# Optimization experiments

Measured on AMD Instinct MI355X. Metric: run time of the kernel, lower is better.

## Reference

```python
import jax, jax.numpy as jnp
import numpy as np

BS, L, S, AMB = 64, 64, 63, 32   # batch, sentence len, opseq steps, ambiguities per step
H, E, V, MLP = 128, 300, 50000, 1024
EPS = 1e-8


def setup_inputs() -> dict:
    key = jax.random.key(0)
    ks = jax.random.split(key, 12)
    u = lambda k, shp: jax.random.uniform(k, shp, dtype=jnp.float32) * 0.1
    return {
        "sentences1": jax.random.randint(ks[0], (BS, L), 0, V, dtype=jnp.int32),
        "operations1": jax.random.randint(ks[1], (BS, S, 2 * AMB), 0, L, dtype=jnp.int32),
        "oopl1": jnp.full((BS,), L + S, dtype=jnp.int32),
        "sentences2": jax.random.randint(ks[2], (BS, L), 0, V, dtype=jnp.int32),
        "operations2": jax.random.randint(ks[3], (BS, S, 2 * AMB), 0, L, dtype=jnp.int32),
        "oopl2": jnp.full((BS,), L + S, dtype=jnp.int32),
        "W": u(ks[4], (5 * H, E)),
        "U": u(ks[5], (5 * H, 2 * H)),
        "b": jnp.zeros((5 * H,), dtype=jnp.float32),
        "energy_u": u(ks[6], (H,)),
        "unk_embedding": u(ks[7], (E,)),
        "word_embeddings": jax.random.normal(ks[8], (V, E), dtype=jnp.float32),
        "A": u(ks[9], (MLP, 4 * H)),
        "a": u(ks[10], (MLP,)),
        "inv_temperature": jnp.float32(1.0),
    }


def _gates(preact, ccL, ccR):
    # preact: [..., 5H]; tree-LSTM cell (i, fL, fR, o, u gates)
    i = jax.nn.sigmoid(preact[..., :H])
    fL = jax.nn.sigmoid(preact[..., H:2 * H])
    fR = jax.nn.sigmoid(preact[..., 2 * H:3 * H])
    o = jax.nn.sigmoid(preact[..., 3 * H:4 * H])
    u = jnp.tanh(preact[..., 4 * H:5 * H])
    c = fL * ccL + fR * ccR + i * u
    h = o * jnp.tanh(c)
    return c, h


def _run_chart(sentences, operations, W, U, b, energy_u, unk_embedding,
               word_embeddings, inv_temperature):
    bs = sentences.shape[0]
    # leaf phase: embed each word, preact = W @ emb + b, ccL = ccR = 0
    emb = jnp.where(sentences[..., None] >= 0,
                    word_embeddings[jnp.clip(sentences, 0)], unk_embedding)  # [bs,L,E]
    preact = jnp.einsum('ble,ge->blg', emb, W) + b                            # [bs,L,5H]
    c, h = _gates(preact, 0.0, 0.0)
    chart = jnp.zeros((bs, L + S, 2 * H), dtype=jnp.float32)
    chart = chart.at[:, :L, :].set(jnp.concatenate([c, h], axis=-1))

    def step(chart, inp):
        ops, pos = inp                                   # ops: [bs, 2*AMB], pos: scalar
        entries = jnp.take_along_axis(chart, ops[:, :, None].astype(jnp.int32), axis=1)
        entries = entries.reshape(bs, AMB, 2, 2 * H)     # [bs, amb, (L,R), 2H]
        ccL = entries[:, :, 0, :H]
        ccR = entries[:, :, 1, :H]
        hh = entries[:, :, :, H:].reshape(bs, AMB, 2 * H)  # concat(hL, hR)
        pre = jnp.einsum('bak,gk->bag', hh, U) + b         # [bs, amb, 5H]
        c, h = _gates(pre, ccL, ccR)
        # cosine similarity of h against energy_u
        hn = jnp.maximum(jnp.sqrt(jnp.sum(h * h, axis=-1)), EPS)
        un = jnp.maximum(jnp.sqrt(jnp.sum(energy_u * energy_u)), EPS)
        e = jnp.einsum('bah,h->ba', h, energy_u) / (hn * un)
        s = jax.nn.softmax(e * inv_temperature, axis=1)    # [bs, amb]
        combined = jnp.concatenate([jnp.einsum('ba,bah->bh', s, c),
                                    jnp.einsum('ba,bah->bh', s, h)], axis=-1)
        chart = jax.lax.dynamic_update_slice(chart, combined[:, None, :], (0, pos, 0))
        return chart, None

    ops_seq = jnp.swapaxes(operations, 0, 1)             # [S, bs, 2*AMB]
    positions = L + jnp.arange(S, dtype=jnp.int32)
    chart, _ = jax.lax.scan(step, chart, (ops_seq, positions))
    return chart


def reference(sentences1, operations1, oopl1, sentences2, operations2, oopl2,
              W, U, b, energy_u, unk_embedding, word_embeddings, A, a,
              inv_temperature):
    chart1 = _run_chart(sentences1, operations1, W, U, b, energy_u,
                        unk_embedding, word_embeddings, inv_temperature)
    chart2 = _run_chart(sentences2, operations2, W, U, b, energy_u,
                        unk_embedding, word_embeddings, inv_temperature)
    bs = chart1.shape[0]
    bidx = jnp.arange(bs)
    s1 = chart1[bidx, oopl1 - 1, H:]                     # final composed h, [bs, H]
    s2 = chart2[bidx, oopl2 - 1, H:]
    u = (s1 - s2) ** 2
    v = s1 * s2
    conc = jnp.concatenate([u, v, s1, s2], axis=1)       # [bs, 4H]
    out = jax.nn.relu(jnp.einsum('jk,ik->ij', A, conc) + a)
    return out
```

## Files before the change

kernel.cpp:

```cpp
#include <hip/hip_runtime.h>
#include <hip/hip_bf16.h>

#define BSZ 64
#define LL  64
#define SS  63
#define AMB 32
#define HH  128
#define EE  300
#define MLPN 1024
#define GG  640
#define K2  256
#define PP  127
#define CCS 36

typedef __attribute__((ext_vector_type(8))) short short8;
typedef __attribute__((ext_vector_type(4))) float f32x4;

__device__ __forceinline__ float sigf(float x) { return 1.f / (1.f + __expf(-x)); }

__device__ __forceinline__ unsigned short f2bf(float x) {
    unsigned int u = __float_as_uint(x);
    u += 0x7fffu + ((u >> 16) & 1u);
    return (unsigned short)(u >> 16);
}

#define PW 25600
#define PU 20480
#define PZ 129024
__global__ void __launch_bounds__(256) prep_kernel(
        const float* __restrict__ W, const float* __restrict__ U,
        const int* __restrict__ ops1, const int* __restrict__ ops2,
        const int* __restrict__ oopl1, const int* __restrict__ oopl2,
        short* __restrict__ WTB, short* __restrict__ UTB,
        float* __restrict__ chart,
        int* __restrict__ live_list, int* __restrict__ nlive_bar) {
    __shared__ unsigned char live[2][64];
    const int tid = threadIdx.x;

    if (blockIdx.x == gridDim.x - 1) {
        if (tid < 128) live[tid >> 6][tid & 63] = 0;
        __syncthreads();
        if (tid < BSZ) {
            int p1 = oopl1[tid] - 1;
            if (p1 >= LL && p1 < PP) live[0][p1 - LL] = 1;
            int p2 = oopl2[tid] - 1;
            if (p2 >= LL && p2 < PP) live[1][p2 - LL] = 1;
        }
        __syncthreads();
        for (int t = SS - 1; t >= 1; --t) {
            if (live[0][t]) {
                for (int i = tid; i < BSZ * 2 * AMB; i += 256) {
                    int p = ops1[((i >> 6) * SS + t) * 64 + (i & 63)];
                    if (p >= LL && p < PP) live[0][p - LL] = 1;
                }
            }
            if (live[1][t]) {
                for (int i = tid; i < BSZ * 2 * AMB; i += 256) {
                    int p = ops2[((i >> 6) * SS + t) * 64 + (i & 63)];
                    if (p >= LL && p < PP) live[1][p - LL] = 1;
                }
            }
            __syncthreads();
        }
        if (tid == 0) {
            int n = 0;
            for (int t = 0; t < SS; ++t) {
                int f = (live[0][t] ? 1 : 0) | (live[1][t] ? 2 : 0);
                if (f) live_list[n++] = t | (f << 8);
            }
            nlive_bar[0] = n;
            nlive_bar[1] = 0;
        }
        return;
    }

    int idx = blockIdx.x * 256 + tid;
    if (idx < PW) {
        int lane = idx & 63, r = idx >> 6;
        int kk = r % 10, n = r / 10;
        int g = n * 16 + (lane & 15);
        int k0 = kk * 32 + ((lane >> 4) << 3);
        const float* src = W + (size_t)g * EE + k0;
        float f[8];
        if (k0 + 8 <= EE) {
            f32x4 x0 = *(const f32x4*)src;
            f32x4 x1 = *(const f32x4*)(src + 4);
            f[0]=x0[0]; f[1]=x0[1]; f[2]=x0[2]; f[3]=x0[3];
            f[4]=x1[0]; f[5]=x1[1]; f[6]=x1[2]; f[7]=x1[3];
        } else {
#pragma unroll
            for (int j = 0; j < 8; ++j) f[j] = (k0 + j < EE) ? src[j] : 0.f;
        }
        short8 v;
#pragma unroll
        for (int j = 0; j < 8; ++j) v[j] = (short)f2bf(f[j]);
        *(short8*)(WTB + (size_t)idx * 8) = v;
    } else if (idx < PW + PU) {
        int o = idx - PW;
        int lane = o & 63, r = o >> 6;
        int kk = r & 7, n = r >> 3;
        int g = n * 16 + (lane & 15);
        int k0 = kk * 32 + ((lane >> 4) << 3);
        const float* src = U + (size_t)g * K2 + k0;
        f32x4 x0 = *(const f32x4*)src;
        f32x4 x1 = *(const f32x4*)(src + 4);
        short8 v;
        v[0]=(short)f2bf(x0[0]); v[1]=(short)f2bf(x0[1]); v[2]=(short)f2bf(x0[2]); v[3]=(short)f2bf(x0[3]);
        v[4]=(short)f2bf(x1[0]); v[5]=(short)f2bf(x1[1]); v[6]=(short)f2bf(x1[2]); v[7]=(short)f2bf(x1[3]);
        *(short8*)(UTB + (size_t)o * 8) = v;
    } else if (idx < PW + PU + PZ) {
        int z = idx - PW - PU;
        int row = z >> 4;
        int pair = row / 63, srow = row - pair * 63;
        float* p = chart + ((size_t)pair * PP + LL + srow) * K2 + ((z & 15) << 4);
        f32x4 zero = {0.f, 0.f, 0.f, 0.f};
        *(f32x4*)p = zero; *(f32x4*)(p+4) = zero; *(f32x4*)(p+8) = zero; *(f32x4*)(p+12) = zero;
    }
}

__global__ void __launch_bounds__(256) leaf_kernel(
        const int* __restrict__ sent1, const int* __restrict__ sent2,
        const short* __restrict__ WTB, const float* __restrict__ bias,
        const float* __restrict__ unk, const float* __restrict__ wemb,
        float* __restrict__ chart) {
    __shared__ short8 As[2 * 10 * 64];
    const int tid  = threadIdx.x;
    const int tok0 = blockIdx.x * 32;
    const int* sent = (blockIdx.x >= 128) ? sent2 : sent1;

    float f[5][8];
    int ts[5], os[5];
#pragma unroll
    for (int i = 0; i < 5; ++i) {
        int slot = i * 256 + tid;
        int t = slot / 40, oct = slot - t * 40;
        ts[i] = t; os[i] = oct;
        int s = sent[(tok0 + t) & 4095];
        const float* src = (s >= 0) ? (wemb + (size_t)s * EE) : unk;
        int k0 = oct * 8;
        if (k0 + 8 <= EE) {
            f32x4 x0 = *(const f32x4*)(src + k0);
            f32x4 x1 = *(const f32x4*)(src + k0 + 4);
            f[i][0]=x0[0]; f[i][1]=x0[1]; f[i][2]=x0[2]; f[i][3]=x0[3];
            f[i][4]=x1[0]; f[i][5]=x1[1]; f[i][6]=x1[2]; f[i][7]=x1[3];
        } else {
#pragma unroll
            for (int j = 0; j < 8; ++j) f[i][j] = (k0 + j < EE) ? src[k0 + j] : 0.f;
        }
    }
#pragma unroll
    for (int i = 0; i < 5; ++i) {
        int t = ts[i], oct = os[i];
        short8 v;
#pragma unroll
        for (int j = 0; j < 8; ++j) v[j] = (short)f2bf(f[i][j]);
        As[((t >> 4) * 10 + (oct >> 2)) * 64 + ((oct & 3) << 4) + (t & 15)] = v;
    }
    __syncthreads();

    const int w = tid >> 6, lane = tid & 63;
    const int quad = lane >> 4, l15 = lane & 15;
    for (int cc = 0; cc < 2; ++cc) {
        int nu = cc * 4 + w;
        f32x4 acc[2][3] = {};
        for (int kk = 0; kk < 10; ++kk) {
            short8 a0 = As[kk * 64 + lane];
            short8 a1 = As[(10 + kk) * 64 + lane];
#pragma unroll
            for (int si = 0; si < 3; ++si) {
                int s5 = (si == 0) ? 0 : (si == 1 ? 3 : 4);
                short8 bv = *(const short8*)(WTB + ((size_t)((nu + 8 * s5) * 10 + kk) * 64 + lane) * 8);
                acc[0][si] = __builtin_amdgcn_mfma_f32_16x16x32_bf16(a0, bv, acc[0][si], 0, 0, 0);
                acc[1][si] = __builtin_amdgcn_mfma_f32_16x16x32_bf16(a1, bv, acc[1][si], 0, 0, 0);
            }
        }
        int jc = nu * 16 + l15;
        float bi = bias[jc], bo = bias[384 + jc], bu = bias[512 + jc];
#pragma unroll
        for (int mt = 0; mt < 2; ++mt)
#pragma unroll
        for (int r = 0; r < 4; ++r) {
            float pi = acc[mt][0][r] + bi;
            float po = acc[mt][1][r] + bo;
            float pu = acc[mt][2][r] + bu;
            float cv = sigf(pi) * tanhf(pu);
            float hv = sigf(po) * tanhf(cv);
            int tok = tok0 + mt * 16 + quad * 4 + r;
            float* dst = chart + ((size_t)(tok >> 6) * PP + (tok & 63)) * K2;
            dst[jc]      = cv;
            dst[HH + jc] = hv;
        }
    }
}

#define GRID_STEP 512
__device__ __forceinline__ void gbar(int* bar, int gen) {
    __syncthreads();
    if (threadIdx.x == 0) {
        __threadfence();
        __hip_atomic_fetch_add(bar, 1, __ATOMIC_ACQ_REL, __HIP_MEMORY_SCOPE_AGENT);
        while (__hip_atomic_load(bar, __ATOMIC_ACQUIRE, __HIP_MEMORY_SCOPE_AGENT) < gen * GRID_STEP)
            __builtin_amdgcn_s_sleep(2);
        __threadfence();
    }
    __syncthreads();
}

__global__ void __launch_bounds__(256, 2) step_kernel(
        const int* __restrict__ ops1, const int* __restrict__ ops2,
        const short* __restrict__ UTB, const float* __restrict__ bias,
        const float* __restrict__ eu, const float* __restrict__ invt,
        float* __restrict__ chart,
        const int* __restrict__ live_list, int* __restrict__ nlive_bar,
        float* __restrict__ e_scr) {
    __shared__ __align__(16) char smem[16384 + 4 * (32 * CCS * 4)];
    short8* As2 = (short8*)smem;
    float* ccL = (float*)(smem + 16384);
    float* ccR = (float*)(smem + 16384 + 4608);
    float* chc = (float*)(smem + 16384 + 2 * 4608);
    float* chh = (float*)(smem + 16384 + 3 * 4608);
    __shared__ int ops_lds[64];
    __shared__ float s_w[AMB];
    __shared__ float un_sh;

    const int tid = threadIdx.x;
    const int pair = blockIdx.x >> 2, slice = blockIdx.x & 3;
    const int ch = pair >> 6, b = pair & 63;
    const int* ops = ch ? ops2 : ops1;
    float* chbase = chart + (size_t)pair * PP * K2;
    const float it = invt[0];
    const int w = tid >> 6, lane = tid & 63, quad = lane >> 4, l15 = lane & 15;
    const int mt = w >> 1, nul = w & 1, nu = slice * 2 + nul;
    const int jc = nu * 16 + l15, lc = nul * 16 + l15;
    const float bi  = bias[jc],          bfl = bias[HH + jc];
    const float bfr = bias[2 * HH + jc], bo  = bias[3 * HH + jc];
    const float bu  = bias[4 * HH + jc];
    const float euc = eu[slice * 32 + (lane & 31)];

    if (tid < 64) {
        float v = eu[tid] * eu[tid] + eu[tid + 64] * eu[tid + 64];
        for (int off = 32; off >= 1; off >>= 1) v += __shfl_xor(v, off);
        if (tid == 0) un_sh = fmaxf(sqrtf(v), 1e-8f);
    }
    __syncthreads();

    const int nl = nlive_bar[0];
    int* bar = nlive_bar + 1;
    int gen = 0;

    for (int sidx = 0; sidx < nl; ++sidx) {
        int entry = live_list[sidx];
        int t = entry & 0xff;
        bool active = (entry >> (8 + ch)) & 1;

        if (active) {
            if (tid < 64) ops_lds[tid] = min(max(ops[(b * SS + t) * 64 + tid], 0), PP - 1);
            __syncthreads();

            float hf[4][8];
            int ha[4], ho[4];
#pragma unroll
            for (int i = 0; i < 4; ++i) {
                int s = i * 256 + tid;
                int a = s >> 5, oct = s & 31, side = oct >> 4, m8 = oct & 15;
                ha[i] = a; ho[i] = oct;
                const float* src = chbase + (size_t)ops_lds[2 * a + side] * K2 + HH + m8 * 8;
                f32x4 x0 = *(const f32x4*)src;
                f32x4 x1 = *(const f32x4*)(src + 4);
                hf[i][0]=x0[0]; hf[i][1]=x0[1]; hf[i][2]=x0[2]; hf[i][3]=x0[3];
                hf[i][4]=x1[0]; hf[i][5]=x1[1]; hf[i][6]=x1[2]; hf[i][7]=x1[3];
            }
            f32x4 cv4[2];
            int ca[2], cq[2], cs[2];
#pragma unroll
            for (int i = 0; i < 2; ++i) {
                int s2 = i * 256 + tid;
                int a = s2 >> 4, rest = s2 & 15, side = rest >> 3, qi = rest & 7;
                ca[i] = a; cq[i] = qi; cs[i] = side;
                cv4[i] = *(const f32x4*)(chbase + (size_t)ops_lds[2 * a + side] * K2 + slice * 32 + qi * 4);
            }
#pragma unroll
            for (int i = 0; i < 4; ++i) {
                short8 v;
#pragma unroll
                for (int j = 0; j < 8; ++j) v[j] = (short)f2bf(hf[i][j]);
                As2[((ha[i] >> 4) * 8 + (ho[i] >> 2)) * 64 + ((ho[i] & 3) << 4) + (ha[i] & 15)] = v;
            }
#pragma unroll
            for (int i = 0; i < 2; ++i) {
                float* dst = (cs[i] ? ccR : ccL) + ca[i] * CCS + cq[i] * 4;
                *(f32x4*)dst = cv4[i];
            }
            __syncthreads();

            f32x4 acc[5] = {};
            for (int kk = 0; kk < 8; ++kk) {
                short8 a0 = As2[(mt * 8 + kk) * 64 + lane];
#pragma unroll
                for (int s5 = 0; s5 < 5; ++s5) {
                    short8 bb = *(const short8*)(UTB + ((size_t)((nu + 8 * s5) * 8 + kk) * 64 + lane) * 8);
                    acc[s5] = __builtin_amdgcn_mfma_f32_16x16x32_bf16(a0, bb, acc[s5], 0, 0, 0);
                }
            }
#pragma unroll
            for (int r = 0; r < 4; ++r) {
                int a = mt * 16 + quad * 4 + r;
                float cv = sigf(acc[1][r] + bfl) * ccL[a * CCS + lc]
                         + sigf(acc[2][r] + bfr) * ccR[a * CCS + lc]
                         + sigf(acc[0][r] + bi) * tanhf(acc[4][r] + bu);
                float hv = sigf(acc[3][r] + bo) * tanhf(cv);
                chc[a * CCS + lc] = cv;
                chh[a * CCS + lc] = hv;
            }
            __syncthreads();

#pragma unroll
            for (int ii = 0; ii < 4; ++ii) {
                int a = w * 8 + ii * 2 + (lane >> 5);
                float hv = chh[a * CCS + (lane & 31)];
                float pe = hv * euc, pn = hv * hv;
                for (int off = 16; off >= 1; off >>= 1) {
                    pe += __shfl_xor(pe, off);
                    pn += __shfl_xor(pn, off);
                }
                if ((lane & 31) == 0) {
                    float* d = e_scr + ((size_t)(pair * 4 + slice) * 32 + a) * 2;
                    d[0] = pe; d[1] = pn;
                }
            }
        }

        ++gen; gbar(bar, gen);

        if (active) {
            if (tid < 32) {
                const float* es = e_scr + (size_t)pair * 256 + tid * 2;
                float num = es[0] + es[64] + es[128] + es[192];
                float h2  = es[1] + es[65] + es[129] + es[193];
                float v = (num / (fmaxf(sqrtf(h2), 1e-8f) * un_sh)) * it;
                float m = v;
                for (int off = 16; off >= 1; off >>= 1) m = fmaxf(m, __shfl_xor(m, off));
                float ex = __expf(v - m);
                float su = ex;
                for (int off = 16; off >= 1; off >>= 1) su += __shfl_xor(su, off);
                s_w[tid] = ex / su;
            }
            __syncthreads();
            if (tid < 64) {
                int half = tid >> 5, lcc = tid & 31;
                const float* srcA = half ? chh : chc;
                float sacc = 0.f;
#pragma unroll
                for (int a = 0; a < AMB; ++a) sacc = fmaf(s_w[a], srcA[a * CCS + lcc], sacc);
                chbase[(size_t)(LL + t) * K2 + half * HH + slice * 32 + lcc] = sacc;
            }
            __syncthreads();
        }

        if (sidx + 1 < nl) { ++gen; gbar(bar, gen); }
    }
}

__global__ void __launch_bounds__(256) mlp_kernel(
        const float* __restrict__ chart,
        const int* __restrict__ oopl1, const int* __restrict__ oopl2,
        const float* __restrict__ A, const float* __restrict__ abias,
        float* __restrict__ out) {
    __shared__ __align__(16) float conc[4][512];
    const int tid = threadIdx.x;
    const int jt = blockIdx.x & 15, bt = blockIdx.x >> 4;

#pragma unroll
    for (int i = 0; i < 2; ++i) {
        int s = i * 256 + tid;
        int bl = s >> 7, kv = s & 127;
        int k0 = kv * 4, sel = k0 >> 7, kk0 = k0 & 127;
        int b = bt * 4 + bl;
        int p1 = min(max(oopl1[b] - 1, 0), PP - 1);
        int p2 = min(max(oopl2[b] - 1, 0), PP - 1);
        f32x4 s1 = *(const f32x4*)(chart + ((size_t)(b * PP + p1)) * K2 + HH + kk0);
        f32x4 s2 = *(const f32x4*)(chart + ((size_t)((BSZ + b) * PP + p2)) * K2 + HH + kk0);
        f32x4 v;
        if (sel == 0)      { f32x4 d = s1 - s2; v = d * d; }
        else if (sel == 1) v = s1 * s2;
        else if (sel == 2) v = s1;
        else               v = s2;
        *(f32x4*)&conc[bl][k0] = v;
    }
    __syncthreads();

    const int jj = tid & 63, bg = tid >> 6;
    const int j = jt * 64 + jj, b = bt * 4 + bg;
    const float* Arow = A + (size_t)j * 512;
    float acc0 = abias[j], acc1 = 0.f;
    for (int k = 0; k < 512; k += 8) {
        f32x4 a0 = *(const f32x4*)(Arow + k);
        f32x4 a1 = *(const f32x4*)(Arow + k + 4);
        f32x4 c0 = *(const f32x4*)&conc[bg][k];
        f32x4 c1 = *(const f32x4*)&conc[bg][k + 4];
#pragma unroll
        for (int u = 0; u < 4; ++u) {
            acc0 = fmaf(a0[u], c0[u], acc0);
            acc1 = fmaf(a1[u], c1[u], acc1);
        }
    }
    out[(size_t)b * MLPN + j] = fmaxf(acc0 + acc1, 0.f);
}

extern "C" void kernel_launch(void* const* d_in, const int* in_sizes, int n_in,
                              void* d_out, int out_size, void* d_ws, size_t ws_size,
                              hipStream_t stream) {
    const int*   sent1 = (const int*)d_in[0];
    const int*   ops1  = (const int*)d_in[1];
    const int*   oopl1 = (const int*)d_in[2];
    const int*   sent2 = (const int*)d_in[3];
    const int*   ops2  = (const int*)d_in[4];
    const int*   oopl2 = (const int*)d_in[5];
    const float* W     = (const float*)d_in[6];
    const float* U     = (const float*)d_in[7];
    const float* bias  = (const float*)d_in[8];
    const float* eu    = (const float*)d_in[9];
    const float* unk   = (const float*)d_in[10];
    const float* wemb  = (const float*)d_in[11];
    const float* A     = (const float*)d_in[12];
    const float* ab    = (const float*)d_in[13];
    const float* invt  = (const float*)d_in[14];
    float* out = (float*)d_out;
    (void)in_sizes; (void)n_in; (void)out_size; (void)ws_size;

    char* ws = (char*)d_ws;
    const size_t CHART_OFF = 0;
    const size_t WTB_OFF   = 16646144;
    const size_t UTB_OFF   = 17055744;
    const size_t LIST_OFF  = 17383424;
    const size_t NB_OFF    = 17383680;
    const size_t ESCR_OFF  = 17383936;
    float* chart     = (float*)(ws + CHART_OFF);
    short* WTB       = (short*)(ws + WTB_OFF);
    short* UTB       = (short*)(ws + UTB_OFF);
    int*   live_list = (int*)(ws + LIST_OFF);
    int*   nlive_bar = (int*)(ws + NB_OFF);
    float* e_scr     = (float*)(ws + ESCR_OFF);

    prep_kernel<<<685, 256, 0, stream>>>(W, U, ops1, ops2, oopl1, oopl2,
                                         WTB, UTB, chart, live_list, nlive_bar);

    leaf_kernel<<<256, 256, 0, stream>>>(sent1, sent2, WTB, bias, unk, wemb, chart);

    step_kernel<<<GRID_STEP, 256, 0, stream>>>(ops1, ops2, UTB, bias, eu, invt, chart,
                                               live_list, nlive_bar, e_scr);

    mlp_kernel<<<256, 256, 0, stream>>>(chart, oopl1, oopl2, A, ab, out);
}
```

Before: 214.0 us.

## Fuse leaf and step phases into one per-pair block, drop grid barriers

Replaces the leaf kernel and the grid-barrier step kernel with a single 1024-thread block per sentence pair that computes leaves, zeroes its chart rows, and runs the composition steps with only block-level syncs. Liveness analysis now runs per batch element with a 64-bit mask inside each block, rather than as a union across the batch in the prep kernel. This removes the cross-block atomic barriers and scratch traffic for the energy reduction. In exchange only 128 blocks run, so much of the GPU sits idle and each block's serial step chain is longer.

```diff
diff --git a/kernel.cpp b/kernel.cpp
--- a/kernel.cpp
+++ b/kernel.cpp
@@ -11,7 +11,6 @@
 #define GG  640
 #define K2  256
 #define PP  127
-#define CCS 36
 
 typedef __attribute__((ext_vector_type(8))) short short8;
 typedef __attribute__((ext_vector_type(4))) float f32x4;
@@ -26,55 +25,10 @@
 
 #define PW 25600
 #define PU 20480
-#define PZ 129024
 __global__ void __launch_bounds__(256) prep_kernel(
         const float* __restrict__ W, const float* __restrict__ U,
-        const int* __restrict__ ops1, const int* __restrict__ ops2,
-        const int* __restrict__ oopl1, const int* __restrict__ oopl2,
-        short* __restrict__ WTB, short* __restrict__ UTB,
-        float* __restrict__ chart,
-        int* __restrict__ live_list, int* __restrict__ nlive_bar) {
-    __shared__ unsigned char live[2][64];
-    const int tid = threadIdx.x;
-
-    if (blockIdx.x == gridDim.x - 1) {
-        if (tid < 128) live[tid >> 6][tid & 63] = 0;
-        __syncthreads();
-        if (tid < BSZ) {
-            int p1 = oopl1[tid] - 1;
-            if (p1 >= LL && p1 < PP) live[0][p1 - LL] = 1;
-            int p2 = oopl2[tid] - 1;
-            if (p2 >= LL && p2 < PP) live[1][p2 - LL] = 1;
-        }
-        __syncthreads();
-        for (int t = SS - 1; t >= 1; --t) {
-            if (live[0][t]) {
-                for (int i = tid; i < BSZ * 2 * AMB; i += 256) {
-                    int p = ops1[((i >> 6) * SS + t) * 64 + (i & 63)];
-                    if (p >= LL && p < PP) live[0][p - LL] = 1;
-                }
-            }
-            if (live[1][t]) {
-                for (int i = tid; i < BSZ * 2 * AMB; i += 256) {
-                    int p = ops2[((i >> 6) * SS + t) * 64 + (i & 63)];
-                    if (p >= LL && p < PP) live[1][p - LL] = 1;
-                }
-            }
-            __syncthreads();
-        }
-        if (tid == 0) {
-            int n = 0;
-            for (int t = 0; t < SS; ++t) {
-                int f = (live[0][t] ? 1 : 0) | (live[1][t] ? 2 : 0);
-                if (f) live_list[n++] = t | (f << 8);
-            }
-            nlive_bar[0] = n;
-            nlive_bar[1] = 0;
-        }
-        return;
-    }
-
-    int idx = blockIdx.x * 256 + tid;
+        short* __restrict__ WTB, short* __restrict__ UTB) {
+    int idx = blockIdx.x * 256 + threadIdx.x;
     if (idx < PW) {
         int lane = idx & 63, r = idx >> 6;
         int kk = r % 10, n = r / 10;
@@ -108,256 +62,232 @@
         v[0]=(short)f2bf(x0[0]); v[1]=(short)f2bf(x0[1]); v[2]=(short)f2bf(x0[2]); v[3]=(short)f2bf(x0[3]);
         v[4]=(short)f2bf(x1[0]); v[5]=(short)f2bf(x1[1]); v[6]=(short)f2bf(x1[2]); v[7]=(short)f2bf(x1[3]);
         *(short8*)(UTB + (size_t)o * 8) = v;
-    } else if (idx < PW + PU + PZ) {
-        int z = idx - PW - PU;
-        int row = z >> 4;
-        int pair = row / 63, srow = row - pair * 63;
-        float* p = chart + ((size_t)pair * PP + LL + srow) * K2 + ((z & 15) << 4);
-        f32x4 zero = {0.f, 0.f, 0.f, 0.f};
-        *(f32x4*)p = zero; *(f32x4*)(p+4) = zero; *(f32x4*)(p+8) = zero; *(f32x4*)(p+12) = zero;
-    }
-}
-
-__global__ void __launch_bounds__(256) leaf_kernel(
+    }
+}
+
+__global__ void __launch_bounds__(1024) main_kernel(
         const int* __restrict__ sent1, const int* __restrict__ sent2,
-        const short* __restrict__ WTB, const float* __restrict__ bias,
+        const int* __restrict__ ops1, const int* __restrict__ ops2,
+        const int* __restrict__ oopl1, const int* __restrict__ oopl2,
+        const short* __restrict__ WTB, const short* __restrict__ UTB,
+        const float* __restrict__ bias, const float* __restrict__ eu,
+        const float* __restrict__ invt,
         const float* __restrict__ unk, const float* __restrict__ wemb,
         float* __restrict__ chart) {
-    __shared__ short8 As[2 * 10 * 64];
-    const int tid  = threadIdx.x;
-    const int tok0 = blockIdx.x * 32;
-    const int* sent = (blockIdx.x >= 128) ? sent2 : sent1;
-
-    float f[5][8];
-    int ts[5], os[5];
-#pragma unroll
-    for (int i = 0; i < 5; ++i) {
-        int slot = i * 256 + tid;
-        int t = slot / 40, oct = slot - t * 40;
-        ts[i] = t; os[i] = oct;
-        int s = sent[(tok0 + t) & 4095];
-        const float* src = (s >= 0) ? (wemb + (size_t)s * EE) : unk;
-        int k0 = oct * 8;
-        if (k0 + 8 <= EE) {
-            f32x4 x0 = *(const f32x4*)(src + k0);
-            f32x4 x1 = *(const f32x4*)(src + k0 + 4);
-            f[i][0]=x0[0]; f[i][1]=x0[1]; f[i][2]=x0[2]; f[i][3]=x0[3];
-            f[i][4]=x1[0]; f[i][5]=x1[1]; f[i][6]=x1[2]; f[i][7]=x1[3];
-        } else {
-#pragma unroll
-            for (int j = 0; j < 8; ++j) f[i][j] = (k0 + j < EE) ? src[k0 + j] : 0.f;
-        }
-    }
-#pragma unroll
-    for (int i = 0; i < 5; ++i) {
-        int t = ts[i], oct = os[i];
-        short8 v;
-#pragma unroll
-        for (int j = 0; j < 8; ++j) v[j] = (short)f2bf(f[i][j]);
-        As[((t >> 4) * 10 + (oct >> 2)) * 64 + ((oct & 3) << 4) + (t & 15)] = v;
-    }
-    __syncthreads();
-
-    const int w = tid >> 6, lane = tid & 63;
-    const int quad = lane >> 4, l15 = lane & 15;
-    for (int cc = 0; cc < 2; ++cc) {
-        int nu = cc * 4 + w;
-        f32x4 acc[2][3] = {};
-        for (int kk = 0; kk < 10; ++kk) {
-            short8 a0 = As[kk * 64 + lane];
-            short8 a1 = As[(10 + kk) * 64 + lane];
-#pragma unroll
-            for (int si = 0; si < 3; ++si) {
-                int s5 = (si == 0) ? 0 : (si == 1 ? 3 : 4);
-                short8 bv = *(const short8*)(WTB + ((size_t)((nu + 8 * s5) * 10 + kk) * 64 + lane) * 8);
-                acc[0][si] = __builtin_amdgcn_mfma_f32_16x16x32_bf16(a0, bv, acc[0][si], 0, 0, 0);
-                acc[1][si] = __builtin_amdgcn_mfma_f32_16x16x32_bf16(a1, bv, acc[1][si], 0, 0, 0);
-            }
-        }
-        int jc = nu * 16 + l15;
-        float bi = bias[jc], bo = bias[384 + jc], bu = bias[512 + jc];
-#pragma unroll
-        for (int mt = 0; mt < 2; ++mt)
-#pragma unroll
-        for (int r = 0; r < 4; ++r) {
-            float pi = acc[mt][0][r] + bi;
-            float po = acc[mt][1][r] + bo;
-            float pu = acc[mt][2][r] + bu;
-            float cv = sigf(pi) * tanhf(pu);
-            float hv = sigf(po) * tanhf(cv);
-            int tok = tok0 + mt * 16 + quad * 4 + r;
-            float* dst = chart + ((size_t)(tok >> 6) * PP + (tok & 63)) * K2;
-            dst[jc]      = cv;
-            dst[HH + jc] = hv;
-        }
-    }
-}
-
-#define GRID_STEP 512
-__device__ __forceinline__ void gbar(int* bar, int gen) {
-    __syncthreads();
-    if (threadIdx.x == 0) {
-        __threadfence();
-        __hip_atomic_fetch_add(bar, 1, __ATOMIC_ACQ_REL, __HIP_MEMORY_SCOPE_AGENT);
-        while (__hip_atomic_load(bar, __ATOMIC_ACQUIRE, __HIP_MEMORY_SCOPE_AGENT) < gen * GRID_STEP)
-            __builtin_amdgcn_s_sleep(2);
-        __threadfence();
-    }
-    __syncthreads();
-}
-
-__global__ void __launch_bounds__(256, 2) step_kernel(
-        const int* __restrict__ ops1, const int* __restrict__ ops2,
-        const short* __restrict__ UTB, const float* __restrict__ bias,
-        const float* __restrict__ eu, const float* __restrict__ invt,
-        float* __restrict__ chart,
-        const int* __restrict__ live_list, int* __restrict__ nlive_bar,
-        float* __restrict__ e_scr) {
-    __shared__ __align__(16) char smem[16384 + 4 * (32 * CCS * 4)];
-    short8* As2 = (short8*)smem;
-    float* ccL = (float*)(smem + 16384);
-    float* ccR = (float*)(smem + 16384 + 4608);
-    float* chc = (float*)(smem + 16384 + 2 * 4608);
-    float* chh = (float*)(smem + 16384 + 3 * 4608);
+    __shared__ short8 As[40 * 64];
+    __shared__ float chh[32][132];
+    __shared__ float comb[2][2][HH];
     __shared__ int ops_lds[64];
-    __shared__ float s_w[AMB];
+    __shared__ float e_num[AMB], h2s[AMB], s_w[AMB];
+    __shared__ int live_list[SS];
+    __shared__ int nl_sh;
     __shared__ float un_sh;
 
     const int tid = threadIdx.x;
-    const int pair = blockIdx.x >> 2, slice = blockIdx.x & 3;
+    const int pair = blockIdx.x;
     const int ch = pair >> 6, b = pair & 63;
-    const int* ops = ch ? ops2 : ops1;
+    const int* sent = ch ? sent2 : sent1;
+    const int* ops  = ch ? ops2 : ops1;
+    const int* oopl = ch ? oopl2 : oopl1;
     float* chbase = chart + (size_t)pair * PP * K2;
     const float it = invt[0];
     const int w = tid >> 6, lane = tid & 63, quad = lane >> 4, l15 = lane & 15;
-    const int mt = w >> 1, nul = w & 1, nu = slice * 2 + nul;
-    const int jc = nu * 16 + l15, lc = nul * 16 + l15;
-    const float bi  = bias[jc],          bfl = bias[HH + jc];
-    const float bfr = bias[2 * HH + jc], bo  = bias[3 * HH + jc];
-    const float bu  = bias[4 * HH + jc];
-    const float euc = eu[slice * 32 + (lane & 31)];
 
     if (tid < 64) {
         float v = eu[tid] * eu[tid] + eu[tid + 64] * eu[tid + 64];
         for (int off = 32; off >= 1; off >>= 1) v += __shfl_xor(v, off);
         if (tid == 0) un_sh = fmaxf(sqrtf(v), 1e-8f);
+
+        unsigned long long mask = 0ull;
+        int q0 = oopl[b] - 1 - LL;
+        if (q0 >= 0) { if (q0 > SS - 1) q0 = SS - 1; mask = 1ull << q0; }
+        for (int t = SS - 1; t >= 1; --t) {
+            if (mask & (1ull << t)) {
+                int p = ops[(b * SS + t) * 64 + tid];
+                int q = p - LL;
+                unsigned long long bit = (q >= 0 && q < t) ? (1ull << q) : 0ull;
+                for (int off = 32; off >= 1; off >>= 1) bit |= __shfl_xor(bit, off);
+                mask |= bit;
+            }
+        }
+        if (tid == 0) {
+            int n = 0;
+            for (int t = 0; t < SS; ++t)
+                if (mask & (1ull << t)) live_list[n++] = t;
+            nl_sh = n;
+        }
+    }
+
+#pragma unroll
+    for (int i = 0; i < 3; ++i) {
+        int slot = i * 1024 + tid;
+        if (slot < 2560) {
+            int t = slot / 40, oct = slot - t * 40;
+            int s = sent[b * LL + t];
+            const float* src = (s >= 0) ? (wemb + (size_t)s * EE) : unk;
+            int k0 = oct * 8;
+            float f[8];
+            if (k0 + 8 <= EE) {
+                f32x4 x0 = *(const f32x4*)(src + k0);
+                f32x4 x1 = *(const f32x4*)(src + k0 + 4);
+                f[0]=x0[0]; f[1]=x0[1]; f[2]=x0[2]; f[3]=x0[3];
+                f[4]=x1[0]; f[5]=x1[1]; f[6]=x1[2]; f[7]=x1[3];
+            } else {
+#pragma unroll
+                for (int j = 0; j < 8; ++j) f[j] = (k0 + j < EE) ? src[k0 + j] : 0.f;
+            }
+            short8 v;
+#pragma unroll
+            for (int j = 0; j < 8; ++j) v[j] = (short)f2bf(f[j]);
+            As[((t >> 4) * 10 + (oct >> 2)) * 64 + ((oct & 3) << 4) + (t & 15)] = v;
+        }
+    }
+#pragma unroll
+    for (int i = 0; i < 4; ++i) {
+        int off = i * 4096 + tid * 4;
+        if (off < SS * K2) {
+            f32x4 z = {0.f, 0.f, 0.f, 0.f};
+            *(f32x4*)(chbase + (size_t)LL * K2 + off) = z;
+        }
     }
     __syncthreads();
 
-    const int nl = nlive_bar[0];
-    int* bar = nlive_bar + 1;
-    int gen = 0;
+    {
+        const int mt = w & 3, nug = w >> 2;
+        f32x4 acc[2][3] = {};
+        for (int kk = 0; kk < 10; ++kk) {
+            short8 a0 = As[(mt * 10 + kk) * 64 + lane];
+#pragma unroll
+            for (int si = 0; si < 3; ++si) {
+                int s5 = (si == 0) ? 0 : (si == 1 ? 3 : 4);
+#pragma unroll
+                for (int hf = 0; hf < 2; ++hf) {
+                    int n = (nug + hf * 4) + 8 * s5;
+                    short8 bv = *(const short8*)(WTB + ((size_t)(n * 10 + kk) * 64 + lane) * 8);
+                    acc[hf][si] = __builtin_amdgcn_mfma_f32_16x16x32_bf16(a0, bv, acc[hf][si], 0, 0, 0);
+                }
+            }
+        }
+#pragma unroll
+        for (int hf = 0; hf < 2; ++hf) {
+            int jc = (nug + hf * 4) * 16 + l15;
+            float bi = bias[jc], bo = bias[3 * HH + jc], bu = bias[4 * HH + jc];
+#pragma unroll
+            for (int r = 0; r < 4; ++r) {
+                float pi = acc[hf][0][r] + bi;
+                float po = acc[hf][1][r] + bo;
+                float pu = acc[hf][2][r] + bu;
+                float cv = sigf(pi) * tanhf(pu);
+                float hv = sigf(po) * tanhf(cv);
+                int l = mt * 16 + quad * 4 + r;
+                chbase[(size_t)l * K2 + jc]      = cv;
+                chbase[(size_t)l * K2 + HH + jc] = hv;
+            }
+        }
+    }
+    __syncthreads();
+
+    const int nl = nl_sh;
+    const float eul = eu[lane], euh = eu[64 + lane];
+    const int smt = w & 1, snu = w >> 1;
+    const int sjc = snu * 16 + l15;
+    const float bi  = bias[sjc],          bfl = bias[HH + sjc];
+    const float bfr = bias[2 * HH + sjc], bo  = bias[3 * HH + sjc];
+    const float bu  = bias[4 * HH + sjc];
 
     for (int sidx = 0; sidx < nl; ++sidx) {
-        int entry = live_list[sidx];
-        int t = entry & 0xff;
-        bool active = (entry >> (8 + ch)) & 1;
-
-        if (active) {
-            if (tid < 64) ops_lds[tid] = min(max(ops[(b * SS + t) * 64 + tid], 0), PP - 1);
-            __syncthreads();
-
-            float hf[4][8];
-            int ha[4], ho[4];
-#pragma unroll
-            for (int i = 0; i < 4; ++i) {
-                int s = i * 256 + tid;
-                int a = s >> 5, oct = s & 31, side = oct >> 4, m8 = oct & 15;
-                ha[i] = a; ho[i] = oct;
-                const float* src = chbase + (size_t)ops_lds[2 * a + side] * K2 + HH + m8 * 8;
-                f32x4 x0 = *(const f32x4*)src;
-                f32x4 x1 = *(const f32x4*)(src + 4);
-                hf[i][0]=x0[0]; hf[i][1]=x0[1]; hf[i][2]=x0[2]; hf[i][3]=x0[3];
-                hf[i][4]=x1[0]; hf[i][5]=x1[1]; hf[i][6]=x1[2]; hf[i][7]=x1[3];
-            }
-            f32x4 cv4[2];
-            int ca[2], cq[2], cs[2];
-#pragma unroll
-            for (int i = 0; i < 2; ++i) {
-                int s2 = i * 256 + tid;
-                int a = s2 >> 4, rest = s2 & 15, side = rest >> 3, qi = rest & 7;
-                ca[i] = a; cq[i] = qi; cs[i] = side;
-                cv4[i] = *(const f32x4*)(chbase + (size_t)ops_lds[2 * a + side] * K2 + slice * 32 + qi * 4);
-            }
-#pragma unroll
-            for (int i = 0; i < 4; ++i) {
-                short8 v;
-#pragma unroll
-                for (int j = 0; j < 8; ++j) v[j] = (short)f2bf(hf[i][j]);
-                As2[((ha[i] >> 4) * 8 + (ho[i] >> 2)) * 64 + ((ho[i] & 3) << 4) + (ha[i] & 15)] = v;
-            }
-#pragma unroll
-            for (int i = 0; i < 2; ++i) {
-                float* dst = (cs[i] ? ccR : ccL) + ca[i] * CCS + cq[i] * 4;
-                *(f32x4*)dst = cv4[i];
-            }
-            __syncthreads();
-
+        const int t = live_list[sidx];
+        if (tid < 64) ops_lds[tid] = min(max(ops[(b * SS + t) * 64 + tid], 0), PP - 1);
+        __syncthreads();
+
+        {
+            int a = tid >> 5, oct = tid & 31, side = oct >> 4, m8 = oct & 15;
+            const float* src = chbase + (size_t)ops_lds[2 * a + side] * K2 + HH + m8 * 8;
+            f32x4 x0 = *(const f32x4*)src;
+            f32x4 x1 = *(const f32x4*)(src + 4);
+            short8 v;
+            v[0]=(short)f2bf(x0[0]); v[1]=(short)f2bf(x0[1]); v[2]=(short)f2bf(x0[2]); v[3]=(short)f2bf(x0[3]);
+            v[4]=(short)f2bf(x1[0]); v[5]=(short)f2bf(x1[1]); v[6]=(short)f2bf(x1[2]); v[7]=(short)f2bf(x1[3]);
+            As[((a >> 4) * 8 + (oct >> 2)) * 64 + ((oct & 3) << 4) + (a & 15)] = v;
+        }
+        __syncthreads();
+
+        float cvals[4], hvals[4];
+        {
             f32x4 acc[5] = {};
             for (int kk = 0; kk < 8; ++kk) {
-                short8 a0 = As2[(mt * 8 + kk) * 64 + lane];
+                short8 a0 = As[(smt * 8 + kk) * 64 + lane];
 #pragma unroll
                 for (int s5 = 0; s5 < 5; ++s5) {
-                    short8 bb = *(const short8*)(UTB + ((size_t)((nu + 8 * s5) * 8 + kk) * 64 + lane) * 8);
-                    acc[s5] = __builtin_amdgcn_mfma_f32_16x16x32_bf16(a0, bb, acc[s5], 0, 0, 0);
+                    short8 bv = *(const short8*)(UTB + ((size_t)((snu + 8 * s5) * 8 + kk) * 64 + lane) * 8);
+                    acc[s5] = __builtin_amdgcn_mfma_f32_16x16x32_bf16(a0, bv, acc[s5], 0, 0, 0);
                 }
             }
 #pragma unroll
             for (int r = 0; r < 4; ++r) {
-                int a = mt * 16 + quad * 4 + r;
-                float cv = sigf(acc[1][r] + bfl) * ccL[a * CCS + lc]
-                         + sigf(acc[2][r] + bfr) * ccR[a * CCS + lc]
+                int a = smt * 16 + quad * 4 + r;
+                float ccLv = chbase[(size_t)ops_lds[2 * a] * K2 + sjc];
+                float ccRv = chbase[(size_t)ops_lds[2 * a + 1] * K2 + sjc];
+                float cv = sigf(acc[1][r] + bfl) * ccLv
+                         + sigf(acc[2][r] + bfr) * ccRv
                          + sigf(acc[0][r] + bi) * tanhf(acc[4][r] + bu);
                 float hv = sigf(acc[3][r] + bo) * tanhf(cv);
-                chc[a * CCS + lc] = cv;
-                chh[a * CCS + lc] = hv;
-            }
-            __syncthreads();
-
-#pragma unroll
-            for (int ii = 0; ii < 4; ++ii) {
-                int a = w * 8 + ii * 2 + (lane >> 5);
-                float hv = chh[a * CCS + (lane & 31)];
-                float pe = hv * euc, pn = hv * hv;
-                for (int off = 16; off >= 1; off >>= 1) {
-                    pe += __shfl_xor(pe, off);
-                    pn += __shfl_xor(pn, off);
-                }
-                if ((lane & 31) == 0) {
-                    float* d = e_scr + ((size_t)(pair * 4 + slice) * 32 + a) * 2;
-                    d[0] = pe; d[1] = pn;
-                }
-            }
-        }
-
-        ++gen; gbar(bar, gen);
-
-        if (active) {
-            if (tid < 32) {
-                const float* es = e_scr + (size_t)pair * 256 + tid * 2;
-                float num = es[0] + es[64] + es[128] + es[192];
-                float h2  = es[1] + es[65] + es[129] + es[193];
-                float v = (num / (fmaxf(sqrtf(h2), 1e-8f) * un_sh)) * it;
-                float m = v;
-                for (int off = 16; off >= 1; off >>= 1) m = fmaxf(m, __shfl_xor(m, off));
-                float ex = __expf(v - m);
-                float su = ex;
-                for (int off = 16; off >= 1; off >>= 1) su += __shfl_xor(su, off);
-                s_w[tid] = ex / su;
-            }
-            __syncthreads();
-            if (tid < 64) {
-                int half = tid >> 5, lcc = tid & 31;
-                const float* srcA = half ? chh : chc;
-                float sacc = 0.f;
-#pragma unroll
-                for (int a = 0; a < AMB; ++a) sacc = fmaf(s_w[a], srcA[a * CCS + lcc], sacc);
-                chbase[(size_t)(LL + t) * K2 + half * HH + slice * 32 + lcc] = sacc;
-            }
-            __syncthreads();
-        }
-
-        if (sidx + 1 < nl) { ++gen; gbar(bar, gen); }
+                cvals[r] = cv; hvals[r] = hv;
+                chh[a][sjc] = hv;
+            }
+        }
+        __syncthreads();
+
+#pragma unroll
+        for (int i = 0; i < 2; ++i) {
+            int a = w * 2 + i;
+            float h0 = chh[a][lane], h1 = chh[a][64 + lane];
+            float pe = h0 * eul + h1 * euh;
+            float pn = h0 * h0 + h1 * h1;
+            for (int off = 32; off >= 1; off >>= 1) {
+                pe += __shfl_xor(pe, off);
+                pn += __shfl_xor(pn, off);
+            }
+            if (lane == 0) { e_num[a] = pe; h2s[a] = pn; }
+        }
+        __syncthreads();
+
+        if (tid < 64) {
+            float v = (tid < AMB)
+                ? (e_num[tid] / (fmaxf(sqrtf(h2s[tid]), 1e-8f) * un_sh)) * it
+                : -3.4e38f;
+            float m = v;
+            for (int off = 32; off >= 1; off >>= 1) m = fmaxf(m, __shfl_xor(m, off));
+            float ex = (tid < AMB) ? __expf(v - m) : 0.f;
+            float su = ex;
+            for (int off = 32; off >= 1; off >>= 1) su += __shfl_xor(su, off);
+            if (tid < AMB) s_w[tid] = ex / su;
+        }
+        __syncthreads();
+
+        {
+            float sc = 0.f, sh = 0.f;
+#pragma unroll
+            for (int r = 0; r < 4; ++r) {
+                int a = smt * 16 + quad * 4 + r;
+                float sw = s_w[a];
+                sc = fmaf(sw, cvals[r], sc);
+                sh = fmaf(sw, hvals[r], sh);
+            }
+            sc += __shfl_xor(sc, 16); sc += __shfl_xor(sc, 32);
+            sh += __shfl_xor(sh, 16); sh += __shfl_xor(sh, 32);
+            if (lane < 16) {
+                comb[smt][0][sjc] = sc;
+                comb[smt][1][sjc] = sh;
+            }
+        }
+        __syncthreads();
+        if (tid < K2) {
+            int part = tid >> 7, col = tid & 127;
+            float val = comb[0][part][col] + comb[1][part][col];
+            chbase[(size_t)(LL + t) * K2 + part * HH + col] = val;
+        }
+        __syncthreads();
     }
 }
 
@@ -432,23 +362,14 @@
     const size_t CHART_OFF = 0;
     const size_t WTB_OFF   = 16646144;
     const size_t UTB_OFF   = 17055744;
-    const size_t LIST_OFF  = 17383424;
-    const size_t NB_OFF    = 17383680;
-    const size_t ESCR_OFF  = 17383936;
-    float* chart     = (float*)(ws + CHART_OFF);
-    short* WTB       = (short*)(ws + WTB_OFF);
-    short* UTB       = (short*)(ws + UTB_OFF);
-    int*   live_list = (int*)(ws + LIST_OFF);
-    int*   nlive_bar = (int*)(ws + NB_OFF);
-    float* e_scr     = (float*)(ws + ESCR_OFF);
-
-    prep_kernel<<<685, 256, 0, stream>>>(W, U, ops1, ops2, oopl1, oopl2,
-                                         WTB, UTB, chart, live_list, nlive_bar);
-
-    leaf_kernel<<<256, 256, 0, stream>>>(sent1, sent2, WTB, bias, unk, wemb, chart);
-
-    step_kernel<<<GRID_STEP, 256, 0, stream>>>(ops1, ops2, UTB, bias, eu, invt, chart,
-                                               live_list, nlive_bar, e_scr);
+    float* chart = (float*)(ws + CHART_OFF);
+    short* WTB   = (short*)(ws + WTB_OFF);
+    short* UTB   = (short*)(ws + UTB_OFF);
+
+    prep_kernel<<<180, 256, 0, stream>>>(W, U, WTB, UTB);
+
+    main_kernel<<<128, 1024, 0, stream>>>(sent1, sent2, ops1, ops2, oopl1, oopl2,
+                                          WTB, UTB, bias, eu, invt, unk, wemb, chart);
 
     mlp_kernel<<<256, 256, 0, stream>>>(chart, oopl1, oopl2, A, ab, out);
 }
```

Measured after the change: 188.6 us. -11.9%, faster.
